# Kernel tuning notes

Hardware: AMD Instinct MI355X
Metric: run time of the kernel (lower is better)

Reference implementation:

```python
import jax, jax.numpy as jnp
import numpy as np

N = 50000      # nodes
E = 800000     # edges (before self-loops)
D = 128        # input_dim
H = 128        # hidden_dim
G = 256        # graphs in batch


def setup_inputs() -> dict:
    key = jax.random.key(0)
    ks = jax.random.split(key, 6)
    x = jax.random.normal(ks[0], (N, D), dtype=jnp.float32)
    edge_index = jax.random.randint(ks[1], (2, E), 0, N, dtype=jnp.int32)
    batch = jnp.sort(jax.random.randint(ks[2], (N,), 0, G, dtype=jnp.int32))
    W1 = jax.random.normal(ks[3], (D, H), dtype=jnp.float32) / np.sqrt(D).astype(np.float32)
    b1 = jnp.zeros((H,), jnp.float32)
    W2 = jax.random.normal(ks[4], (H, H), dtype=jnp.float32) / np.sqrt(H).astype(np.float32)
    b2 = jnp.zeros((H,), jnp.float32)
    alpha = jnp.full((H,), 0.25, jnp.float32)  # PReLU(hidden_dim) init
    return dict(x=x, edge_index=edge_index, batch=batch,
                W1=W1, b1=b1, W2=W2, b2=b2, alpha=alpha)


def _gcn_layer(z, W, b, src, dst, norm):
    # GCNConv: z' = D^{-1/2}(A+I)D^{-1/2} (z W) + b
    zw = z @ W                                            # [N,H] dense GEMM
    agg = jnp.zeros_like(zw).at[dst].add(norm[:, None] * zw[src])  # scatter-add over edges
    return agg + b


def reference(x, edge_index, batch, W1, b1, W2, b2, alpha):
    loop = jnp.arange(N, dtype=edge_index.dtype)
    src = jnp.concatenate([edge_index[0], loop])          # add self-loops
    dst = jnp.concatenate([edge_index[1], loop])
    deg = jnp.zeros((N,), x.dtype).at[dst].add(jnp.float32(1.0))
    dinv = jnp.where(deg > 0, jax.lax.rsqrt(deg), 0.0)
    norm = dinv[src] * dinv[dst]                          # [E+N] edge weights

    zs = []
    z = x
    for (W, b) in ((W1, b1), (W2, b2)):
        z = _gcn_layer(z, W, b, src, dst, norm)
        z = jnp.where(z > 0, z, alpha * z)                # channel-wise PReLU (shared)
        zs.append(z)

    gs = [jax.ops.segment_sum(zi, batch, num_segments=G) for zi in zs]  # global_add_pool
    g = jnp.concatenate(gs, axis=1)                       # [G, num_layers*H]
    return z, g
```

## Files before the change

kernel.cpp:

```cpp
#include <hip/hip_runtime.h>
#include <stdint.h>


#define CAP 96

typedef __attribute__((ext_vector_type(8))) short short8;
typedef __attribute__((ext_vector_type(4))) float f32x4;

__device__ __forceinline__ uint16_t bf16rne(float f) {
    uint32_t u = __float_as_uint(f);
    uint32_t r = (u + 0x7fffu + ((u >> 16) & 1u)) >> 16;
    return (uint16_t)r;
}
__device__ __forceinline__ float bf_lo(uint32_t v) { return __uint_as_float(v << 16); }
__device__ __forceinline__ float bf_hi(uint32_t v) { return __uint_as_float(v & 0xffff0000u); }

__global__ __launch_bounds__(512) void k0(int* __restrict__ cursor, int nbC, int N,
                                          const float* __restrict__ W1,
                                          const float* __restrict__ W2,
                                          uint16_t* __restrict__ Wf1,
                                          uint16_t* __restrict__ Wf2,
                                          float* __restrict__ g_out, int nbZ,
                                          uint32_t* __restrict__ zw) {
    int bid = blockIdx.x, t = threadIdx.x;
    if (bid < nbC) {
        int i = bid * 512 + t;
        if (i <= N) cursor[i] = 0;
        if (bid == 0 && t < 64) zw[(size_t)N * 64 + t] = 0u;
    } else if (bid < nbC + 8) {
        int tid = (bid - nbC) * 512 + t;
        const float* W = (tid & 2048) ? W2 : W1;
        uint16_t* O = (tid & 2048) ? Wf2 : Wf1;
        int q16 = tid & 2047;
        int lane = q16 & 63, n0ks = q16 >> 6;
        int n0 = n0ks >> 2, ks = n0ks & 3;
        int m = lane & 15, quad = lane >> 4;
        int nn = n0 * 16 + m;
        int kkb = ks * 32 + quad * 8;
        uint16_t v[8];
#pragma unroll
        for (int j = 0; j < 8; ++j) v[j] = bf16rne(W[(kkb + j) * 128 + nn]);
        *(short8*)&O[q16 * 8] = *(short8*)v;
    } else {
        int idx = (bid - nbC - 8) * 512 + t;
        ((float4*)g_out)[idx] = make_float4(0.f, 0.f, 0.f, 0.f);
    }
}

__device__ __forceinline__ void gemm_body(const float* Xf, const uint16_t* Xb,
                                          const uint16_t* __restrict__ Wf,
                                          uint16_t* __restrict__ Y, int nrows,
                                          const int* __restrict__ cnt,
                                          uint16_t* Wl, int bid, int t) {
    int lane = t & 63, w = t >> 6;
    int row0 = bid * 128;
    for (int c = t; c < 2048; c += 512)
        *(short8*)&Wl[c * 8] = *(const short8*)&Wf[c * 8];
    int m = lane & 15, quad = lane >> 4;
    int arow = row0 + w * 16 + m;
    bool rowok = arow < nrows;
    short8 a[4];
    short8 zer = {0, 0, 0, 0, 0, 0, 0, 0};
    if (Xb) {
        const uint16_t* aptr = Xb + (size_t)arow * 128 + quad * 8;
#pragma unroll
        for (int ks = 0; ks < 4; ++ks)
            a[ks] = rowok ? *(const short8*)(aptr + ks * 32) : zer;
    } else {
        const float* ap = Xf + (size_t)arow * 128 + quad * 8;
#pragma unroll
        for (int ks = 0; ks < 4; ++ks) {
            if (rowok) {
                float4 u0 = *(const float4*)(ap + ks * 32);
                float4 u1 = *(const float4*)(ap + ks * 32 + 4);
                uint32_t q[4];
                q[0] = (uint32_t)bf16rne(u0.x) | ((uint32_t)bf16rne(u0.y) << 16);
                q[1] = (uint32_t)bf16rne(u0.z) | ((uint32_t)bf16rne(u0.w) << 16);
                q[2] = (uint32_t)bf16rne(u1.x) | ((uint32_t)bf16rne(u1.y) << 16);
                q[3] = (uint32_t)bf16rne(u1.z) | ((uint32_t)bf16rne(u1.w) << 16);
                a[ks] = *(short8*)q;
            } else a[ks] = zer;
        }
    }
    __syncthreads();

    f32x4 acc[8];
#pragma unroll
    for (int i = 0; i < 8; ++i) acc[i] = (f32x4){0.f, 0.f, 0.f, 0.f};
#pragma unroll
    for (int ks = 0; ks < 4; ++ks)
#pragma unroll
        for (int n0 = 0; n0 < 8; ++n0) {
            short8 b = *(short8*)&Wl[((n0 * 4 + ks) * 64 + lane) * 8];
            acc[n0] = __builtin_amdgcn_mfma_f32_16x16x32_bf16(a[ks], b, acc[n0], 0, 0, 0);
        }
    __syncthreads();

    float dsc[4] = {1.f, 1.f, 1.f, 1.f};
    if (cnt) {
#pragma unroll
        for (int r = 0; r < 4; ++r) {
            int gr = row0 + w * 16 + quad * 4 + r;
            int d = (gr < nrows) ? cnt[gr] : 0;
            dsc[r] = rsqrtf((float)(d + 1));
        }
    }

    uint16_t* Ep = Wl;
#pragma unroll
    for (int n0 = 0; n0 < 8; ++n0)
#pragma unroll
        for (int r = 0; r < 4; ++r)
            Ep[(w * 16 + quad * 4 + r) * 136 + n0 * 16 + m] = bf16rne(acc[n0][r] * dsc[r]);
    for (int r16 = 0; r16 < 16; ++r16) {
        int row = row0 + w * 16 + r16;
        if (row < nrows) {
            uint32_t v = *(uint32_t*)&Ep[(w * 16 + r16) * 136 + lane * 2];
            ((uint32_t*)Y)[(size_t)row * 64 + lane] = v;
        }
    }
}

__device__ __forceinline__ void fill_body(const int* __restrict__ src, const int* __restrict__ dst,
                                          int* __restrict__ cursor, uint16_t* __restrict__ col,
                                          int E, int fb, int t) {
    int base = fb * 1024 + t;
    int d[2], s[2], p[2];
#pragma unroll
    for (int k = 0; k < 2; ++k) {
        int e = base + k * 512;
        d[k] = (e < E) ? dst[e] : -1;
        s[k] = (e < E) ? src[e] : 0;
    }
#pragma unroll
    for (int k = 0; k < 2; ++k) if (d[k] >= 0) p[k] = atomicAdd(&cursor[d[k]], 1);
#pragma unroll
    for (int k = 0; k < 2; ++k)
        if (d[k] >= 0 && p[k] < CAP) col[(size_t)d[k] * CAP + p[k]] = (uint16_t)s[k];
}

__global__ __launch_bounds__(512, 8) void k5(const float* __restrict__ X,
                                             const uint16_t* __restrict__ Wf,
                                             uint16_t* __restrict__ Y, int nrows, int gemmGrid,
                                             const int* __restrict__ src, const int* __restrict__ dst,
                                             int* __restrict__ cursor, uint16_t* __restrict__ col,
                                             int E, int fillGrid) {
    __shared__ uint16_t Wl[17408];
    int bid = blockIdx.x, t = threadIdx.x;
    int mn = min(gemmGrid, fillGrid), mn2 = 2 * mn;
    int role, idx;
    if (bid < mn2) { role = bid & 1; idx = bid >> 1; }
    else { role = (gemmGrid > fillGrid) ? 0 : 1; idx = bid - mn2 + mn; }
    if (role == 0) gemm_body(X, nullptr, Wf, Y, nrows, nullptr, Wl, idx, t);
    else fill_body(src, dst, cursor, col, E, idx, t);
}

__global__ __launch_bounds__(512, 8) void gemm2k(const uint16_t* __restrict__ Xb,
                                                 const uint16_t* __restrict__ Wf,
                                                 uint16_t* __restrict__ Y, int nrows,
                                                 const int* __restrict__ cnt) {
    __shared__ uint16_t Wl[17408];
    gemm_body(nullptr, Xb, Wf, Y, nrows, cnt, Wl, blockIdx.x, threadIdx.x);
}

__global__ __launch_bounds__(512) void zscale(uint32_t* __restrict__ zw,
                                              const int* __restrict__ cnt, int ndw) {
    int idx = blockIdx.x * 512 + threadIdx.x;
    if (idx >= ndw) return;
    int row = idx >> 6;
    float di = rsqrtf((float)(cnt[row] + 1));
    uint32_t v = zw[idx];
    float lo = bf_lo(v) * di, hi = bf_hi(v) * di;
    zw[idx] = (uint32_t)bf16rne(lo) | ((uint32_t)bf16rne(hi) << 16);
}

template <bool PS>
__global__ __launch_bounds__(256) void aggp(const uint32_t* __restrict__ zw,
                                            const int* __restrict__ cnt,
                                            const uint16_t* __restrict__ col,
                                            const float* __restrict__ bias,
                                            const float* __restrict__ alpha,
                                            const int* __restrict__ batch,
                                            float* __restrict__ gout, int col_off,
                                            uint32_t* __restrict__ z1b,
                                            float* __restrict__ zoutf,
                                            int mode, int n) {
    __shared__ float red[4][128];
    int wv = threadIdx.x >> 6;
    int lane = threadIdx.x & 63;
    int c = lane * 2;
    int b0 = blockIdx.x * 16;
    int base = b0 + wv * 4;
    int g0 = batch[min(b0, n - 1)];
    int gL = batch[min(b0 + 15, n - 1)];
    bool uni = (g0 == gL);
    float bsx = bias[c], bsy = bias[c + 1];
    float pax = alpha[c], pay = alpha[c + 1];

    int nd[4], dg[4];
    uint32_t sv[4], cc[4];
#pragma unroll
    for (int q = 0; q < 4; ++q) {
        int node = base + q;
        nd[q] = (node < n) ? node : n;
        dg[q] = cnt[nd[q]];
        sv[q] = zw[(size_t)nd[q] * 64 + lane];
        cc[q] = ((const uint32_t*)(col + (size_t)nd[q] * CAP))[lane < 48 ? lane : 0];
    }

    float psx = 0.f, psy = 0.f;
#pragma unroll
    for (int q = 0; q < 4; ++q) {
        int node = base + q;
        bool valid = node < n;
        float di = rsqrtf((float)(dg[q] + 1));
        float sw = PS ? 1.f : di;
        float ax = sw * bf_lo(sv[q]), ay = sw * bf_hi(sv[q]);
        float bx = 0.f, by = 0.f;
        int len = min(dg[q], CAP);
        int len8 = (len + 7) & ~7;
        for (int e = 0; e < len8; e += 8) {
            int h = e >> 1;
            uint32_t q0 = (uint32_t)__builtin_amdgcn_readlane((int)cc[q], h);
            uint32_t q1 = (uint32_t)__builtin_amdgcn_readlane((int)cc[q], h + 1);
            uint32_t q2 = (uint32_t)__builtin_amdgcn_readlane((int)cc[q], h + 2);
            uint32_t q3 = (uint32_t)__builtin_amdgcn_readlane((int)cc[q], h + 3);
            int s0 = (e + 0 < len) ? (int)(q0 & 0xffffu) : n;
            int s1 = (e + 1 < len) ? (int)(q0 >> 16)     : n;
            int s2 = (e + 2 < len) ? (int)(q1 & 0xffffu) : n;
            int s3 = (e + 3 < len) ? (int)(q1 >> 16)     : n;
            int s4 = (e + 4 < len) ? (int)(q2 & 0xffffu) : n;
            int s5 = (e + 5 < len) ? (int)(q2 >> 16)     : n;
            int s6 = (e + 6 < len) ? (int)(q3 & 0xffffu) : n;
            int s7 = (e + 7 < len) ? (int)(q3 >> 16)     : n;
            uint32_t v0 = zw[(size_t)s0 * 64 + lane];
            uint32_t v1 = zw[(size_t)s1 * 64 + lane];
            uint32_t v2 = zw[(size_t)s2 * 64 + lane];
            uint32_t v3 = zw[(size_t)s3 * 64 + lane];
            uint32_t v4 = zw[(size_t)s4 * 64 + lane];
            uint32_t v5 = zw[(size_t)s5 * 64 + lane];
            uint32_t v6 = zw[(size_t)s6 * 64 + lane];
            uint32_t v7 = zw[(size_t)s7 * 64 + lane];
            float w0 = PS ? 1.f : rsqrtf((float)(cnt[s0] + 1));
            float w1 = PS ? 1.f : rsqrtf((float)(cnt[s1] + 1));
            float w2 = PS ? 1.f : rsqrtf((float)(cnt[s2] + 1));
            float w3 = PS ? 1.f : rsqrtf((float)(cnt[s3] + 1));
            float w4 = PS ? 1.f : rsqrtf((float)(cnt[s4] + 1));
            float w5 = PS ? 1.f : rsqrtf((float)(cnt[s5] + 1));
            float w6 = PS ? 1.f : rsqrtf((float)(cnt[s6] + 1));
            float w7 = PS ? 1.f : rsqrtf((float)(cnt[s7] + 1));
            ax += w0 * bf_lo(v0); ay += w0 * bf_hi(v0);
            bx += w1 * bf_lo(v1); by += w1 * bf_hi(v1);
            ax += w2 * bf_lo(v2); ay += w2 * bf_hi(v2);
            bx += w3 * bf_lo(v3); by += w3 * bf_hi(v3);
            ax += w4 * bf_lo(v4); ay += w4 * bf_hi(v4);
            bx += w5 * bf_lo(v5); by += w5 * bf_hi(v5);
            ax += w6 * bf_lo(v6); ay += w6 * bf_hi(v6);
            bx += w7 * bf_lo(v7); by += w7 * bf_hi(v7);
        }
        ax += bx; ay += by;
        float zx = di * ax + bsx;
        float zy = di * ay + bsy;
        zx = zx > 0.f ? zx : pax * zx;
        zy = zy > 0.f ? zy : pay * zy;

        if (valid) {
            if (mode == 0) {
                uint32_t pk = (uint32_t)bf16rne(zx) | ((uint32_t)bf16rne(zy) << 16);
                z1b[(size_t)node * 64 + lane] = pk;
            } else {
                ((float2*)zoutf)[(size_t)node * 64 + lane] = make_float2(zx, zy);
            }
        }
        float cx = valid ? zx : 0.f, cy = valid ? zy : 0.f;
        if (uni) {
            psx += cx; psy += cy;
        } else if (valid) {
            int gr = batch[node];
            float* bp = &gout[(size_t)gr * 256 + col_off];
            atomicAdd(&bp[c], cx);
            atomicAdd(&bp[c + 1], cy);
        }
    }

    if (uni) {
        red[wv][c] = psx; red[wv][c + 1] = psy;
        __syncthreads();
        if (wv == 0) {
            float sx = red[0][c] + red[1][c] + red[2][c] + red[3][c];
            float sy = red[0][c + 1] + red[1][c + 1] + red[2][c + 1] + red[3][c + 1];
            float* bp = &gout[(size_t)g0 * 256 + col_off];
            atomicAdd(&bp[c], sx);
            atomicAdd(&bp[c + 1], sy);
        }
    }
}

extern "C" void kernel_launch(void* const* d_in, const int* in_sizes, int n_in,
                              void* d_out, int out_size, void* d_ws, size_t ws_size,
                              hipStream_t stream) {
    const float* x     = (const float*)d_in[0];
    const int*   eidx  = (const int*)d_in[1];
    const int*   batch = (const int*)d_in[2];
    const float* W1    = (const float*)d_in[3];
    const float* b1    = (const float*)d_in[4];
    const float* W2    = (const float*)d_in[5];
    const float* b2    = (const float*)d_in[6];
    const float* alpha = (const float*)d_in[7];

    const int N = in_sizes[2];
    const int E = in_sizes[1] / 2;
    const int G = (out_size - N * 128) / 256;

    const int* src = eidx;
    const int* dst = eidx + E;

    char* ws = (char*)d_ws;
    size_t off = 0;
    auto alloc = [&](size_t bytes) { void* q = ws + off; off = (off + bytes + 255) & ~(size_t)255; return q; };
    int*      cursor = (int*)alloc((size_t)(N + 1) * 4);
    uint16_t* col    = (uint16_t*)alloc((size_t)N * CAP * 2);
    uint32_t* zw     = (uint32_t*)alloc((size_t)(N + 1) * 128 * 2);
    uint32_t* z1b    = (uint32_t*)alloc((size_t)N * 128 * 2);
    uint16_t* Wf1    = (uint16_t*)alloc(128 * 128 * 2);
    uint16_t* Wf2    = (uint16_t*)alloc(128 * 128 * 2);

    float* z_out = (float*)d_out;
    float* g_out = (float*)d_out + (size_t)N * 128;

    int nbC      = (N + 512) / 512;
    int nbZ      = (G * 256 / 4 + 511) / 512;
    int fillGrid = (E + 1023) / 1024;
    int gemmGrid = (N + 127) / 128;
    int aggGrid  = (N + 15) / 16;
    int ndw      = N * 64;
    int zsGrid   = (ndw + 511) / 512;

    k0<<<nbC + 8 + nbZ, 512, 0, stream>>>(cursor, nbC, N, W1, W2, Wf1, Wf2, g_out, nbZ, zw);
    k5<<<gemmGrid + fillGrid, 512, 0, stream>>>(x, Wf1, (uint16_t*)zw, N, gemmGrid,
                                                src, dst, cursor, col, E, fillGrid);
    zscale<<<zsGrid, 512, 0, stream>>>(zw, cursor, ndw);
    aggp<true><<<aggGrid, 256, 0, stream>>>(zw, cursor, col, b1, alpha, batch,
                                            g_out, 0, z1b, nullptr, 0, N);
    gemm2k<<<gemmGrid, 512, 0, stream>>>((const uint16_t*)z1b, Wf2, (uint16_t*)zw, N, cursor);
    aggp<true><<<aggGrid, 256, 0, stream>>>(zw, cursor, col, b2, alpha, batch,
                                            g_out, 128, nullptr, z_out, 1, N);
}
```

Before: 210.9 us.

## Partition CSR fill by destination range so each XCD owns one slice

The fused GEMM/fill kernel now maps blocks so that every 9th block does a GEMM tile and the rest do edge fill. Fill blocks are split by block index mod 8, which on MI355X's round-robin dispatch lines up with the XCD. Each fill block scans a 2048-edge chunk but only handles edges whose destination falls in its eighth of the node range. This keeps cursor atomics and col writes for a given node inside one XCD's L2, avoiding cross-die coherence traffic. In exchange every edge index is read eight times, and the mapping relies on the hardware's round-robin block placement.

After: 216.4 us. +2.6%, slower.

```diff
diff --git a/kernel.cpp b/kernel.cpp
--- a/kernel.cpp
+++ b/kernel.cpp
@@ -123,20 +123,23 @@
 
 __device__ __forceinline__ void fill_body(const int* __restrict__ src, const int* __restrict__ dst,
                                           int* __restrict__ cursor, uint16_t* __restrict__ col,
-                                          int E, int fb, int t) {
-    int base = fb * 1024 + t;
-    int d[2], s[2], p[2];
-#pragma unroll
-    for (int k = 0; k < 2; ++k) {
+                                          int E, int sub, int lo, int hi, int t) {
+    int base = sub * 2048 + t;
+    int d[4], s[4], p[4];
+    bool ok[4];
+#pragma unroll
+    for (int k = 0; k < 4; ++k) {
         int e = base + k * 512;
-        d[k] = (e < E) ? dst[e] : -1;
-        s[k] = (e < E) ? src[e] : 0;
-    }
-#pragma unroll
-    for (int k = 0; k < 2; ++k) if (d[k] >= 0) p[k] = atomicAdd(&cursor[d[k]], 1);
-#pragma unroll
-    for (int k = 0; k < 2; ++k)
-        if (d[k] >= 0 && p[k] < CAP) col[(size_t)d[k] * CAP + p[k]] = (uint16_t)s[k];
+        bool v = e < E;
+        d[k] = v ? dst[e] : -1;
+        s[k] = v ? src[e] : 0;
+        ok[k] = v && d[k] >= lo && d[k] < hi;
+    }
+#pragma unroll
+    for (int k = 0; k < 4; ++k) if (ok[k]) p[k] = atomicAdd(&cursor[d[k]], 1);
+#pragma unroll
+    for (int k = 0; k < 4; ++k)
+        if (ok[k] && p[k] < CAP) col[(size_t)d[k] * CAP + p[k]] = (uint16_t)s[k];
 }
 
 __global__ __launch_bounds__(512, 8) void k5(const float* __restrict__ X,
@@ -144,15 +147,26 @@
                                              uint16_t* __restrict__ Y, int nrows, int gemmGrid,
                                              const int* __restrict__ src, const int* __restrict__ dst,
                                              int* __restrict__ cursor, uint16_t* __restrict__ col,
-                                             int E, int fillGrid) {
+                                             int E, int FB) {
     __shared__ uint16_t Wl[17408];
     int bid = blockIdx.x, t = threadIdx.x;
-    int mn = min(gemmGrid, fillGrid), mn2 = 2 * mn;
-    int role, idx;
-    if (bid < mn2) { role = bid & 1; idx = bid >> 1; }
-    else { role = (gemmGrid > fillGrid) ? 0 : 1; idx = bid - mn2 + mn; }
-    if (role == 0) gemm_body(X, nullptr, Wf, Y, nrows, nullptr, Wl, idx, t);
-    else fill_body(src, dst, cursor, col, E, idx, t);
+    int per = bid / 72;
+    int m = bid - per * 72;
+    if (m % 9 == 0) {
+        int idx = bid / 9;
+        if (idx < gemmGrid)
+            gemm_body(X, nullptr, Wf, Y, nrows, nullptr, Wl, idx, t);
+    } else {
+        int r = m & 7;
+        int rank = ((m - r) >> 3) - ((9 * r < m) ? 1 : 0);
+        int sub = per * 8 + rank;
+        if (sub < FB) {
+            int Q = (nrows + 7) >> 3;
+            int lo = r * Q;
+            int hi = min(lo + Q, nrows);
+            fill_body(src, dst, cursor, col, E, sub, lo, hi, t);
+        }
+    }
 }
 
 __global__ __launch_bounds__(512, 8) void gemm2k(const uint16_t* __restrict__ Xb,
@@ -330,15 +344,16 @@
 
     int nbC      = (N + 512) / 512;
     int nbZ      = (G * 256 / 4 + 511) / 512;
-    int fillGrid = (E + 1023) / 1024;
     int gemmGrid = (N + 127) / 128;
+    int FB       = (E + 2047) / 2048;
+    int k5Grid   = 9 * (((FB > gemmGrid) ? FB : gemmGrid) + 1);
     int aggGrid  = (N + 15) / 16;
     int ndw      = N * 64;
     int zsGrid   = (ndw + 511) / 512;
 
     k0<<<nbC + 8 + nbZ, 512, 0, stream>>>(cursor, nbC, N, W1, W2, Wf1, Wf2, g_out, nbZ, zw);
-    k5<<<gemmGrid + fillGrid, 512, 0, stream>>>(x, Wf1, (uint16_t*)zw, N, gemmGrid,
-                                                src, dst, cursor, col, E, fillGrid);
+    k5<<<k5Grid, 512, 0, stream>>>(x, Wf1, (uint16_t*)zw, N, gemmGrid,
+                                   src, dst, cursor, col, E, FB);
     zscale<<<zsGrid, 512, 0, stream>>>(zw, cursor, ndw);
     aggp<true><<<aggGrid, 256, 0, stream>>>(zw, cursor, col, b1, alpha, batch,
                                             g_out, 0, z1b, nullptr, 0, N);
```
